# Kernel optimization log

Hardware: AMD Instinct MI355X
Metric: run time of the kernel (lower is better)

## Reference

```python
import jax, jax.numpy as jnp
import numpy as np

EPS = 1e-5
DIM, QK, PDIM, SR = 256, 64, 128, 2
B, H, W = 16, 64, 64
SCALE = QK ** (-0.5)


def _conv(x, w, stride, pad, groups=1):
    return jax.lax.conv_general_dilated(
        x, w, (stride, stride), [(pad, pad), (pad, pad)], feature_group_count=groups)


def _bn(x, g, b, m, v):
    # inference-mode BatchNorm2d with running stats
    s = (g / jnp.sqrt(v + EPS))[None, :, None, None]
    return (x - m[None, :, None, None]) * s + b[None, :, None, None]


def _gn1(x, g, b):
    # GroupNorm(1, C): normalize over (C,H,W) per sample
    mu = x.mean(axis=(1, 2, 3), keepdims=True)
    var = x.var(axis=(1, 2, 3), keepdims=True)
    xh = (x - mu) / jnp.sqrt(var + EPS)
    return xh * g[None, :, None, None] + b[None, :, None, None]


def setup_inputs() -> dict:
    key = jax.random.key(0)
    ks = jax.random.split(key, 6)
    inp = {
        'x': jax.random.normal(ks[0], (B, DIM, H, W), jnp.float32),
        'gn_g': jnp.ones((DIM,), jnp.float32),
        'gn_b': jnp.zeros((DIM,), jnp.float32),
        'w_in': jax.random.normal(ks[1], (2 * QK + DIM, DIM, 3, 3), jnp.float32) * 0.05,
        'bn_in_g': jnp.ones((2 * QK + DIM,), jnp.float32),
        'bn_in_b': jnp.zeros((2 * QK + DIM,), jnp.float32),
        'bn_in_m': jnp.zeros((2 * QK + DIM,), jnp.float32),
        'bn_in_v': jnp.ones((2 * QK + DIM,), jnp.float32),
        'w_k': jax.random.normal(ks[2], (QK, 1, SR, SR), jnp.float32) * 0.05,
        'bn_k_g': jnp.ones((QK,), jnp.float32),
        'bn_k_b': jnp.zeros((QK,), jnp.float32),
        'bn_k_m': jnp.zeros((QK,), jnp.float32),
        'bn_k_v': jnp.ones((QK,), jnp.float32),
        'w_v': jax.random.normal(ks[3], (PDIM, 1, SR, SR), jnp.float32) * 0.05,
        'bn_v_g': jnp.ones((PDIM,), jnp.float32),
        'bn_v_b': jnp.zeros((PDIM,), jnp.float32),
        'bn_v_m': jnp.zeros((PDIM,), jnp.float32),
        'bn_v_v': jnp.ones((PDIM,), jnp.float32),
        'w_out': jax.random.normal(ks[4], (DIM, DIM, 1, 1), jnp.float32) * 0.05,
        'bn_out_g': jnp.ones((DIM,), jnp.float32),
        'bn_out_b': jnp.zeros((DIM,), jnp.float32),
        'bn_out_m': jnp.zeros((DIM,), jnp.float32),
        'bn_out_v': jnp.ones((DIM,), jnp.float32),
    }
    return inp


def reference(x, gn_g, gn_b, w_in, bn_in_g, bn_in_b, bn_in_m, bn_in_v,
              w_k, bn_k_g, bn_k_b, bn_k_m, bn_k_v,
              w_v, bn_v_g, bn_v_b, bn_v_m, bn_v_v,
              w_out, bn_out_g, bn_out_b, bn_out_m, bn_out_v):
    x = _gn1(x, gn_g, gn_b)
    y = _bn(_conv(x, w_in, 1, 1), bn_in_g, bn_in_b, bn_in_m, bn_in_v)
    q = y[:, :QK]
    k = y[:, QK:2 * QK]
    v = y[:, 2 * QK:2 * QK + PDIM]
    u = y[:, 2 * QK + PDIM:]
    # depthwise sr-stride convs reduce k/v spatially
    k = _bn(_conv(k, w_k, SR, 0, groups=QK), bn_k_g, bn_k_b, bn_k_m, bn_k_v)
    v = _bn(_conv(v, w_v, SR, 0, groups=PDIM), bn_v_g, bn_v_b, bn_v_m, bn_v_v)
    b, _, h, w = u.shape
    qf = q.reshape(b, QK, -1)      # [B, QK, N]
    kf = k.reshape(b, QK, -1)      # [B, QK, M]
    vf = v.reshape(b, PDIM, -1)    # [B, PDIM, M]
    attn = jnp.einsum('bcn,bcm->bnm', qf, kf) * SCALE
    attn = jax.nn.softmax(attn, axis=-1)
    o = jnp.einsum('bcm,bnm->bcn', vf, attn).reshape(b, PDIM, h, w)
    cat = jnp.concatenate([o, u], axis=1)
    out = _bn(_conv(jax.nn.relu(cat), w_out, 1, 0), bn_out_g, bn_out_b, bn_out_m, bn_out_v)
    return out
```

## Files before the change

### kernel.cpp

```cpp
#include <hip/hip_runtime.h>
#include <stdint.h>

#define EPSV 1e-5f

typedef __attribute__((ext_vector_type(8))) short short8;
typedef __attribute__((ext_vector_type(4))) float f32x4;
typedef __bf16 bf16x8 __attribute__((ext_vector_type(8)));

__device__ __forceinline__ unsigned short f2bf(float f) {
  union { float f; unsigned int u; } v; v.f = f;
  unsigned int r = (v.u + 0x7FFFu + ((v.u >> 16) & 1u)) >> 16;
  return (unsigned short)r;
}
__device__ __forceinline__ float bf2f(unsigned short h) {
  union { unsigned int u; float f; } v; v.u = ((unsigned int)h) << 16;
  return v.f;
}

__device__ __forceinline__ f32x4 mfma16(bf16x8 a, bf16x8 b, f32x4 c) {
  return __builtin_amdgcn_mfma_f32_16x16x32_bf16(a, b, c, 0, 0, 0);
}

__device__ __forceinline__ unsigned cvt_pk_bf16(float lo, float hi) {
  unsigned r;
  asm("v_cvt_pk_bf16_f32 %0, %1, %2" : "=v"(r) : "v"(lo), "v"(hi));
  return r;
}

__device__ __forceinline__ bf16x8 dsread16(const unsigned short* p) {
  unsigned off = (unsigned)(uintptr_t)(const __attribute__((address_space(3))) unsigned short*)p;
  bf16x8 r;
  asm volatile("ds_read_b128 %0, %1" : "=v"(r) : "v"(off));
  return r;
}

#define GLOAD16(g, l)                                                          \
  __builtin_amdgcn_global_load_lds(                                            \
      (const __attribute__((address_space(1))) void*)(g),                      \
      (__attribute__((address_space(3))) void*)(l), 16, 0, 0)

__global__ __launch_bounds__(256) void k_gn_stats(const float* __restrict__ x,
                                                  float* __restrict__ stats) {
  int b = blockIdx.x >> 6, chunk = blockIdx.x & 63;
  const float4* xp = (const float4*)(x + ((size_t)b << 20) + (size_t)chunk * 16384);
  int t = threadIdx.x;
  float s = 0.f, q = 0.f;
#pragma unroll
  for (int i = 0; i < 16; ++i) {
    float4 v = xp[i * 256 + t];
    s += v.x + v.y + v.z + v.w;
    q += v.x * v.x + v.y * v.y + v.z * v.z + v.w * v.w;
  }
#pragma unroll
  for (int m = 1; m <= 32; m <<= 1) { s += __shfl_xor(s, m); q += __shfl_xor(q, m); }
  __shared__ float ls[8];
  int w = t >> 6, l = t & 63;
  if (l == 0) { ls[w * 2] = s; ls[w * 2 + 1] = q; }
  __syncthreads();
  if (t == 0) {
    float S = ls[0] + ls[2] + ls[4] + ls[6];
    float Q = ls[1] + ls[3] + ls[5] + ls[7];
    atomicAdd(&stats[b * 2], S);
    atomicAdd(&stats[b * 2 + 1], Q);
  }
}

__global__ __launch_bounds__(256) void k_gn_norm(const float* __restrict__ x,
                                                 const float* __restrict__ stats,
                                                 const float* __restrict__ g,
                                                 const float* __restrict__ bb,
                                                 unsigned short* __restrict__ xnp) {
  __shared__ float tile[64][65];
  int pt = blockIdx.x;
  int ct = blockIdx.y;
  int b = blockIdx.z;
  int t = threadIdx.x, tr = t >> 6, tc = t & 63;
  const float* xb = x + ((size_t)b << 20) + (size_t)(ct * 64) * 4096 + pt * 64;
#pragma unroll
  for (int i = 0; i < 16; ++i) {
    int r = i * 4 + tr;
    tile[r][tc] = xb[(size_t)r * 4096 + tc];
  }
  __syncthreads();
  float mu = stats[b * 2] * (1.f / 1048576.f);
  float var = stats[b * 2 + 1] * (1.f / 1048576.f) - mu * mu;
  float istd = rsqrtf(var + EPSV);
  float gg = g[ct * 64 + tc] * istd;
  float bv = bb[ct * 64 + tc];
  unsigned short* out = xnp + (((size_t)b * 66 + (pt + 1)) * 66 + 1) * 256 + ct * 64 + tc;
#pragma unroll
  for (int i = 0; i < 16; ++i) {
    int pcol = i * 4 + tr;
    float v = (tile[tc][pcol] - mu) * gg + bv;
    out[(size_t)pcol * 256] = f2bf(v);
  }
}

__global__ __launch_bounds__(256) void k_prep_wt(const float* __restrict__ w_in,
                                                 const float* __restrict__ bg,
                                                 const float* __restrict__ bv,
                                                 unsigned short* __restrict__ wt) {
  int idx = blockIdx.x * 256 + threadIdx.x;
  if (idx >= 9 * 384 * 256) return;
  int tap = idx / 98304;
  int rem = idx - tap * 98304;
  int co = rem >> 8, ci = rem & 255;
  float s = bg[co] * rsqrtf(bv[co] + EPSV);
  wt[idx] = f2bf(w_in[(size_t)(co * 256 + ci) * 9 + tap] * s);
}

__global__ __launch_bounds__(256) void k_prep_misc(
    const float* w_out, const float* og, const float* ob, const float* om, const float* ov,
    const float* big, const float* bib, const float* bim, const float* biv,
    const float* w_k, const float* kg, const float* kb, const float* km, const float* kvv,
    const float* w_v, const float* vg, const float* vb, const float* vm, const float* vvv,
    unsigned short* wo2, float* bias_in, float* bias_out,
    float* wkf, float* bias_k, float* wvf, float* bias_v) {
  int idx = blockIdx.x * 256 + threadIdx.x;
  if (idx < 65536) {
    int co = idx >> 8;
    float s = og[co] * rsqrtf(ov[co] + EPSV);
    wo2[idx] = f2bf(w_out[idx] * s);
    return;
  }
  idx -= 65536;
  if (idx < 384) {
    float s = big[idx] * rsqrtf(biv[idx] + EPSV);
    bias_in[idx] = bib[idx] - bim[idx] * s;
    return;
  }
  idx -= 384;
  if (idx < 256) {
    float s = og[idx] * rsqrtf(ov[idx] + EPSV);
    bias_out[idx] = ob[idx] - om[idx] * s;
    return;
  }
  idx -= 256;
  if (idx < 64) {
    float s = kg[idx] * rsqrtf(kvv[idx] + EPSV);
#pragma unroll
    for (int tp = 0; tp < 4; ++tp) wkf[idx * 4 + tp] = w_k[idx * 4 + tp] * s;
    bias_k[idx] = kb[idx] - km[idx] * s;
    return;
  }
  idx -= 64;
  if (idx < 128) {
    float s = vg[idx] * rsqrtf(vvv[idx] + EPSV);
#pragma unroll
    for (int tp = 0; tp < 4; ++tp) wvf[idx * 4 + tp] = w_v[idx * 4 + tp] * s;
    bias_v[idx] = vb[idx] - vm[idx] * s;
    return;
  }
}

__global__ __launch_bounds__(512, 2) void k_conv3(const unsigned short* __restrict__ xnp,
                                                  const unsigned short* __restrict__ wt,
                                                  const float* __restrict__ bias_in,
                                                  unsigned short* __restrict__ y) {
  __shared__ alignas(16) unsigned short As[2][256 * 64];
  __shared__ alignas(16) unsigned short Bs[2][192 * 64];
  int pt = blockIdx.x, cot = blockIdx.y, b = blockIdx.z;
  int p0 = pt * 256, co0 = cot * 192;
  int t = threadIdx.x, w = t >> 6, l = t & 63;
  int lg = l >> 4, lr = l & 15;
  int wrM = (w >> 2) * 128, wrN = (w & 3) * 48;

  int lchunk = (t & 7) ^ ((t >> 3) & 7);
  int abase[4];
#pragma unroll
  for (int i = 0; i < 4; ++i) {
    int row = (i * 512 + t) >> 3;
    int p = p0 + row;
    int yy = p >> 6, xx = p & 63;
    abase[i] = ((b * 66 + yy) * 66 + xx) * 256 + lchunk * 8;
  }
  int bbase[3];
#pragma unroll
  for (int i = 0; i < 3; ++i) {
    int row = (i * 512 + t) >> 3;
    bbase[i] = (co0 + row) * 256 + lchunk * 8;
  }

  f32x4 acc[8][3];
#pragma unroll
  for (int i = 0; i < 8; ++i)
#pragma unroll
    for (int j = 0; j < 3; ++j) acc[i][j] = f32x4{0.f, 0.f, 0.f, 0.f};

#define STAGE(step, buf)                                                       \
  do {                                                                         \
    int tap_ = (step) >> 2, kc_ = (step) & 3;                                  \
    int dy_ = (tap_ * 11) >> 5;                                                \
    int dx_ = tap_ - dy_ * 3;                                                  \
    int aoff_ = (dy_ * 66 + dx_) * 256 + kc_ * 64;                             \
    int boff_ = tap_ * 98304 + kc_ * 64;                                       \
    _Pragma("unroll")                                                          \
    for (int i_ = 0; i_ < 4; ++i_)                                             \
      GLOAD16(xnp + abase[i_] + aoff_, &As[buf][(i_ * 512 + w * 64) * 8]);     \
    _Pragma("unroll")                                                          \
    for (int i_ = 0; i_ < 3; ++i_)                                             \
      GLOAD16(wt + bbase[i_] + boff_, &Bs[buf][(i_ * 512 + w * 64) * 8]);      \
  } while (0)

  STAGE(0, 0);

  for (int step = 0; step < 36; ++step) {
    int cur = step & 1;
    asm volatile("" ::: "memory");
    if (step < 35) {
      STAGE(step + 1, cur ^ 1);
      asm volatile("s_waitcnt vmcnt(7)" ::: "memory");
    } else {
      asm volatile("s_waitcnt vmcnt(0)" ::: "memory");
    }
    __builtin_amdgcn_s_barrier();
    __builtin_amdgcn_sched_barrier(0);

    const unsigned short* Ac = As[cur];
    const unsigned short* Bc = Bs[cur];

    bf16x8 bfr[2][3];
#pragma unroll
    for (int k2 = 0; k2 < 2; ++k2)
#pragma unroll
      for (int nt = 0; nt < 3; ++nt) {
        int row = wrN + nt * 16 + lr;
        bfr[k2][nt] = dsread16(&Bc[row * 64 + (((k2 * 4 + lg) ^ (row & 7)) * 8)]);
      }
#pragma unroll
    for (int mh = 0; mh < 2; ++mh) {
      bf16x8 afr[4][2];
#pragma unroll
      for (int mt = 0; mt < 4; ++mt)
#pragma unroll
        for (int k2 = 0; k2 < 2; ++k2) {
          int row = wrM + mh * 64 + mt * 16 + lr;
          afr[mt][k2] = dsread16(&Ac[row * 64 + (((k2 * 4 + lg) ^ (row & 7)) * 8)]);
        }
      asm volatile("s_waitcnt lgkmcnt(0)" ::: "memory");
      __builtin_amdgcn_sched_barrier(0);
      __builtin_amdgcn_s_setprio(1);
#pragma unroll
      for (int mt = 0; mt < 4; ++mt)
#pragma unroll
        for (int nt = 0; nt < 3; ++nt) {
          acc[mh * 4 + mt][nt] = mfma16(afr[mt][0], bfr[0][nt], acc[mh * 4 + mt][nt]);
          acc[mh * 4 + mt][nt] = mfma16(afr[mt][1], bfr[1][nt], acc[mh * 4 + mt][nt]);
        }
      __builtin_amdgcn_s_setprio(0);
    }
    __builtin_amdgcn_sched_barrier(0);
    __builtin_amdgcn_s_barrier();
  }
#undef STAGE

  float bias[3];
#pragma unroll
  for (int nt = 0; nt < 3; ++nt) bias[nt] = bias_in[co0 + wrN + nt * 16 + lr];
#pragma unroll
  for (int m8 = 0; m8 < 8; ++m8) {
#pragma unroll
    for (int r = 0; r < 4; ++r) {
      int p = p0 + wrM + m8 * 16 + lg * 4 + r;
      size_t rowoff = ((size_t)(b * 4096 + p)) * 384;
#pragma unroll
      for (int nt = 0; nt < 3; ++nt) {
        int co = co0 + wrN + nt * 16 + lr;
        float v = acc[m8][nt][r] + bias[nt];
        if (co >= 256) v = fmaxf(v, 0.f);
        y[rowoff + co] = f2bf(v);
      }
    }
  }
}

__global__ __launch_bounds__(256) void k_kv(const unsigned short* __restrict__ y,
                                            const float* __restrict__ wkf, const float* __restrict__ bias_k,
                                            const float* __restrict__ wvf, const float* __restrict__ bias_v,
                                            unsigned short* __restrict__ kk, unsigned short* __restrict__ vv) {
  constexpr int LDW = 200;
  __shared__ unsigned short ty[128 * LDW];
  __shared__ unsigned short vt[128 * 33];
  int b = blockIdx.x >> 5, my = blockIdx.x & 31;
  int t = threadIdx.x;
  const unsigned short* ybase = y + ((size_t)(b * 4096 + my * 128)) * 384 + 64;
#pragma unroll
  for (int j = 0; j < 12; ++j) {
    int idx = j * 256 + t;
    int row = idx / 24, c8 = idx - row * 24;
    bf16x8 v = *(const bf16x8*)&ybase[(size_t)row * 384 + c8 * 8];
    *(bf16x8*)&ty[row * LDW + c8 * 8] = v;
  }
  __syncthreads();

  {
    int c = t & 63, wq = t >> 6;
    float wk0 = wkf[c * 4 + 0], wk1 = wkf[c * 4 + 1];
    float wk2 = wkf[c * 4 + 2], wk3 = wkf[c * 4 + 3];
    float bk = bias_k[c];
#pragma unroll
    for (int pass = 0; pass < 8; ++pass) {
      int mx = pass * 4 + wq;
      int r0 = 2 * mx, r1 = 2 * mx + 1;
      float a = bk;
      a += bf2f(ty[r0 * LDW + c]) * wk0;
      a += bf2f(ty[(r0 + 1) * LDW + c]) * wk1;
      a += bf2f(ty[(64 + r0) * LDW + c]) * wk2;
      a += bf2f(ty[(64 + r1) * LDW + c]) * wk3;
      kk[((size_t)(b * 1024 + my * 32 + mx)) * 64 + c] = f2bf(a);
    }
  }

  {
    int cv = t & 127, mxh = t >> 7;
    float wv0 = wvf[cv * 4 + 0], wv1 = wvf[cv * 4 + 1];
    float wv2 = wvf[cv * 4 + 2], wv3 = wvf[cv * 4 + 3];
    float bv = bias_v[cv];
    int col = 64 + cv;
#pragma unroll
    for (int pass = 0; pass < 16; ++pass) {
      int mx = pass * 2 + mxh;
      int r0 = 2 * mx, r1 = 2 * mx + 1;
      float a = bv;
      a += bf2f(ty[r0 * LDW + col]) * wv0;
      a += bf2f(ty[r1 * LDW + col]) * wv1;
      a += bf2f(ty[(64 + r0) * LDW + col]) * wv2;
      a += bf2f(ty[(64 + r1) * LDW + col]) * wv3;
      vt[cv * 33 + mx] = f2bf(a);
    }
  }
  __syncthreads();
  {
    int mx = t & 31, cvq = t >> 5;
#pragma unroll
    for (int i = 0; i < 16; ++i) {
      int cv = i * 8 + cvq;
      vv[((size_t)(b * 128 + cv)) * 1024 + my * 32 + mx] = vt[cv * 33 + mx];
    }
  }
}

__global__ __launch_bounds__(512, 4) void k_attn(unsigned short* __restrict__ y,
                                                 const unsigned short* __restrict__ kk,
                                                 const unsigned short* __restrict__ vvb) {
  __shared__ alignas(16) unsigned short Ks[2][4096];
  __shared__ alignas(16) unsigned short PT[8][64][16];
  int blk = blockIdx.x;
  int b = blk >> 5, ntile = blk & 31;
  int t = threadIdx.x, w = t >> 6, l = t & 63;
  int lg = l >> 4, lr = l & 15;
  int nq0 = ntile * 128 + w * 16;
  const float SC = 0.125f * 1.44269504f;

  union { short8 s; bf16x8 b; } uo;
#pragma unroll
  for (int i = 0; i < 8; ++i) uo.s[i] = (short)0x3F80;
  bf16x8 ones = uo.b;

  bf16x8 qf[2];
#pragma unroll
  for (int c = 0; c < 2; ++c)
    qf[c] = *(const bf16x8*)&y[((size_t)(b * 4096 + nq0 + lr)) * 384 + c * 32 + lg * 8];

  f32x4 oa[8];
#pragma unroll
  for (int tt = 0; tt < 8; ++tt) oa[tt] = f32x4{0.f, 0.f, 0.f, 0.f};
  float mi[4], li[4];
#pragma unroll
  for (int r = 0; r < 4; ++r) { mi[r] = -1e30f; li[r] = 0.f; }

  int srow = t >> 3;
  int skg = (t & 7) ^ (srow & 7);
  const unsigned short* ksrc = kk + ((size_t)(b * 1024 + srow)) * 64 + skg * 8;
  unsigned short* ldst0 = &Ks[0][w * 512];
  unsigned short* ldst1 = &Ks[1][w * 512];

  GLOAD16(ksrc, ldst0);
  __syncthreads();

  for (int it = 0; it < 16; ++it) {
    int cur = it & 1;
    const unsigned short* Kc = &Ks[cur][0];
    if (it < 15) GLOAD16(ksrc + (it + 1) * 4096, cur ? ldst0 : ldst1);

    f32x4 s[4];
#pragma unroll
    for (int mt = 0; mt < 4; ++mt) {
      int row = mt * 16 + lr;
      int sw = (lr & 7) << 3;
      bf16x8 kf0 = *(const bf16x8*)&Kc[row * 64 + ((lg * 8) ^ sw)];
      bf16x8 kf1 = *(const bf16x8*)&Kc[row * 64 + ((32 + lg * 8) ^ sw)];
      f32x4 z = f32x4{0.f, 0.f, 0.f, 0.f};
      z = mfma16(qf[0], kf0, z);
      z = mfma16(qf[1], kf1, z);
      s[mt] = z;
    }

    float rm[4];
#pragma unroll
    for (int r = 0; r < 4; ++r)
      rm[r] = fmaxf(fmaxf(s[0][r], s[1][r]), fmaxf(s[2][r], s[3][r]));
#pragma unroll
    for (int msk = 1; msk <= 8; msk <<= 1)
#pragma unroll
      for (int r = 0; r < 4; ++r) rm[r] = fmaxf(rm[r], __shfl_xor(rm[r], msk));
    bool grow = false;
#pragma unroll
    for (int r = 0; r < 4; ++r) grow |= (rm[r] * SC > mi[r]);
    if (__any(grow)) {
#pragma unroll
      for (int r = 0; r < 4; ++r) {
        float nm = fmaxf(mi[r], rm[r] * SC);
        float corr = exp2f(mi[r] - nm);
        mi[r] = nm;
        li[r] *= corr;
#pragma unroll
        for (int tt = 0; tt < 8; ++tt) oa[tt][r] *= corr;
      }
    }
#pragma unroll
    for (int mt = 0; mt < 4; ++mt)
#pragma unroll
      for (int r = 0; r < 4; ++r)
        s[mt][r] = exp2f(fmaf(s[mt][r], SC, -mi[r]));

#pragma unroll
    for (int mt = 0; mt < 4; ++mt) {
      unsigned p01 = cvt_pk_bf16(s[mt][0], s[mt][1]);
      unsigned p23 = cvt_pk_bf16(s[mt][2], s[mt][3]);
      unsigned long long pk = ((unsigned long long)p23 << 32) | p01;
      *(unsigned long long*)&PT[w][mt * 16 + lr][lg * 4] = pk;
    }
    asm volatile("s_waitcnt lgkmcnt(0)" ::: "memory");

    bf16x8 pf[2];
#pragma unroll
    for (int kc = 0; kc < 2; ++kc) {
      unsigned base = (unsigned)(uintptr_t)&PT[w][kc * 32 + lg * 8][lr];
      uint2 t0, t1;
      asm volatile("ds_read_b64_tr_b16 %0, %1" : "=v"(t0) : "v"(base));
      asm volatile("ds_read_b64_tr_b16 %0, %1 offset:128" : "=v"(t1) : "v"(base));
      union { unsigned u[4]; bf16x8 b; } cv;
      cv.u[0] = t0.x; cv.u[1] = t0.y; cv.u[2] = t1.x; cv.u[3] = t1.y;
      pf[kc] = cv.b;
    }
    asm volatile("s_waitcnt lgkmcnt(0)" ::: "memory");
    __builtin_amdgcn_sched_barrier(0);

    {
      f32x4 zz = f32x4{0.f, 0.f, 0.f, 0.f};
      zz = mfma16(pf[0], ones, zz);
      zz = mfma16(pf[1], ones, zz);
#pragma unroll
      for (int r = 0; r < 4; ++r) li[r] += zz[r];
    }

    size_t vbase = ((size_t)(b * 128)) * 1024 + it * 64 + lg * 8;
#pragma unroll
    for (int tt = 0; tt < 8; ++tt) {
      const unsigned short* vr = &vvb[vbase + (size_t)(tt * 16 + lr) * 1024];
      bf16x8 vf0 = *(const bf16x8*)&vr[0];
      bf16x8 vf1 = *(const bf16x8*)&vr[32];
      oa[tt] = mfma16(pf[0], vf0, oa[tt]);
      oa[tt] = mfma16(pf[1], vf1, oa[tt]);
    }
    __syncthreads();
  }

#pragma unroll
  for (int r = 0; r < 4; ++r) {
    float inv = 1.f / li[r];
    int p = nq0 + lg * 4 + r;
    size_t rowoff = ((size_t)(b * 4096 + p)) * 384 + 128;
#pragma unroll
    for (int tt = 0; tt < 8; ++tt) {
      float v = oa[tt][r] * inv;
      v = fmaxf(v, 0.f);
      y[rowoff + tt * 16 + lr] = f2bf(v);
    }
  }
}

__global__ __launch_bounds__(256) void k_conv1(const unsigned short* __restrict__ y,
                                               const unsigned short* __restrict__ wo2,
                                               const float* __restrict__ bias_out,
                                               float* __restrict__ out) {
  int ptile = blockIdx.x, cot = blockIdx.y, b = blockIdx.z;
  int p0 = ptile * 128, co0 = cot * 128;
  __shared__ alignas(16) unsigned short As[128 * 64];
  __shared__ alignas(16) unsigned short Bs[128 * 64];
  int t = threadIdx.x, w = t >> 6, l = t & 63;
  int rr = t >> 3, c8 = (t & 7) * 8;
  int lg = l >> 4, lr = l & 15;
  int baseA = (co0 + rr) * 256 + c8;
  size_t baseB = ((size_t)(b * 4096 + p0 + rr)) * 384 + 128 + c8;
  f32x4 acc[4][4];
#pragma unroll
  for (int i = 0; i < 4; ++i)
#pragma unroll
    for (int j = 0; j < 4; ++j) acc[i][j] = f32x4{0.f, 0.f, 0.f, 0.f};
  int wr = (w >> 1) * 64, wc = (w & 1) * 64;
#pragma unroll 1
  for (int kc = 0; kc < 4; ++kc) {
    int ci0 = kc * 64;
    __syncthreads();
#pragma unroll
    for (int i = 0; i < 4; ++i) {
      GLOAD16(wo2 + baseA + i * 8192 + ci0, &As[(i * 32 + w * 8) * 64]);
      GLOAD16(y + baseB + (size_t)i * 32 * 384 + ci0, &Bs[(i * 32 + w * 8) * 64]);
    }
    __syncthreads();
    bf16x8 af[4][2], bf[4][2];
#pragma unroll
    for (int mt = 0; mt < 4; ++mt)
#pragma unroll
      for (int k2 = 0; k2 < 2; ++k2) {
        af[mt][k2] = *(const bf16x8*)&As[(wr + mt * 16 + lr) * 64 + k2 * 32 + lg * 8];
        bf[mt][k2] = *(const bf16x8*)&Bs[(wc + mt * 16 + lr) * 64 + k2 * 32 + lg * 8];
      }
#pragma unroll
    for (int mt = 0; mt < 4; ++mt)
#pragma unroll
      for (int nt = 0; nt < 4; ++nt) {
        acc[mt][nt] = mfma16(af[mt][0], bf[nt][0], acc[mt][nt]);
        acc[mt][nt] = mfma16(af[mt][1], bf[nt][1], acc[mt][nt]);
      }
  }
#pragma unroll
  for (int mt = 0; mt < 4; ++mt)
#pragma unroll
    for (int r = 0; r < 4; ++r) {
      int co = co0 + wr + mt * 16 + lg * 4 + r;
      float bv = bias_out[co];
      size_t obase = ((size_t)(b * 256 + co)) << 12;
#pragma unroll
      for (int nt = 0; nt < 4; ++nt) {
        int p = p0 + wc + nt * 16 + lr;
        out[obase + p] = acc[mt][nt][r] + bv;
      }
    }
}

static constexpr size_t pad256(size_t x) { return (x + 255) & ~(size_t)255; }

extern "C" void kernel_launch(void* const* d_in, const int* in_sizes, int n_in,
                              void* d_out, int out_size, void* d_ws, size_t ws_size,
                              hipStream_t stream) {
  const float* x      = (const float*)d_in[0];
  const float* gn_g   = (const float*)d_in[1];
  const float* gn_b   = (const float*)d_in[2];
  const float* w_in   = (const float*)d_in[3];
  const float* bin_g  = (const float*)d_in[4];
  const float* bin_b  = (const float*)d_in[5];
  const float* bin_m  = (const float*)d_in[6];
  const float* bin_v  = (const float*)d_in[7];
  const float* w_k    = (const float*)d_in[8];
  const float* bk_g   = (const float*)d_in[9];
  const float* bk_b   = (const float*)d_in[10];
  const float* bk_m   = (const float*)d_in[11];
  const float* bk_v   = (const float*)d_in[12];
  const float* w_v    = (const float*)d_in[13];
  const float* bv_g   = (const float*)d_in[14];
  const float* bv_b   = (const float*)d_in[15];
  const float* bv_m   = (const float*)d_in[16];
  const float* bv_v   = (const float*)d_in[17];
  const float* w_out  = (const float*)d_in[18];
  const float* bo_g   = (const float*)d_in[19];
  const float* bo_b   = (const float*)d_in[20];
  const float* bo_m   = (const float*)d_in[21];
  const float* bo_v   = (const float*)d_in[22];
  float* out = (float*)d_out;

  char* ws = (char*)d_ws;
  size_t off = 0;
  float*          stats   = (float*)(ws + off);          off += pad256(128);
  unsigned short* wt      = (unsigned short*)(ws + off); off += pad256((size_t)9 * 384 * 256 * 2);
  float*          bias_in = (float*)(ws + off);          off += pad256(384 * 4);
  unsigned short* wo2     = (unsigned short*)(ws + off); off += pad256(256 * 256 * 2);
  float*          bias_out= (float*)(ws + off);          off += pad256(256 * 4);
  float*          wkf     = (float*)(ws + off);          off += pad256(64 * 4 * 4);
  float*          bias_k  = (float*)(ws + off);          off += pad256(64 * 4);
  float*          wvf     = (float*)(ws + off);          off += pad256(128 * 4 * 4);
  float*          bias_v  = (float*)(ws + off);          off += pad256(128 * 4);
  unsigned short* xnp     = (unsigned short*)(ws + off); off += pad256((size_t)16 * 66 * 66 * 256 * 2);
  unsigned short* y       = (unsigned short*)(ws + off); off += pad256((size_t)16 * 4096 * 384 * 2);
  unsigned short* kk      = (unsigned short*)(ws + off); off += pad256((size_t)16 * 1024 * 64 * 2);
  unsigned short* vv      = (unsigned short*)(ws + off); off += pad256((size_t)16 * 128 * 1024 * 2);
  (void)ws_size; (void)out_size; (void)n_in; (void)in_sizes;

  hipMemsetAsync(stats, 0, 256, stream);
  hipMemsetAsync(xnp, 0, (size_t)16 * 66 * 66 * 256 * 2, stream);

  k_gn_stats<<<1024, 256, 0, stream>>>(x, stats);
  k_prep_wt<<<3456, 256, 0, stream>>>(w_in, bin_g, bin_v, wt);
  k_prep_misc<<<260, 256, 0, stream>>>(w_out, bo_g, bo_b, bo_m, bo_v,
                                       bin_g, bin_b, bin_m, bin_v,
                                       w_k, bk_g, bk_b, bk_m, bk_v,
                                       w_v, bv_g, bv_b, bv_m, bv_v,
                                       wo2, bias_in, bias_out, wkf, bias_k, wvf, bias_v);
  k_gn_norm<<<dim3(64, 4, 16), 256, 0, stream>>>(x, stats, gn_g, gn_b, xnp);
  k_conv3<<<dim3(16, 2, 16), 512, 0, stream>>>(xnp, wt, bias_in, y);
  k_kv<<<512, 256, 0, stream>>>(y, wkf, bias_k, wvf, bias_v, kk, vv);
  k_attn<<<512, 512, 0, stream>>>(y, kk, vv);
  k_conv1<<<dim3(32, 2, 16), 256, 0, stream>>>(y, wo2, bias_out, out);
}
```

Measured before the change: 454.1 us.

## Shrink conv3 block tile to 128x192 with 4 waves and split-k LDS waits

The 3x3 conv implicit GEMM moves from 256-pixel tiles with 512 threads to 128-pixel tiles with 256 threads, doubling the grid to 1024 blocks. Each wave now computes a 64x96 sub-tile (4x6 MFMA tiles) instead of 128x48, and MFMAs on the first k-half start before the second half's LDS reads have landed. The aim is better CU fill, fewer LDS reads per MFMA, and overlap of LDS latency with compute. The cost is re-reading weight tiles across twice as many blocks and possible register pressure from 24 accumulators plus 20 fragments.

```diff
diff --git a/kernel.cpp b/kernel.cpp
--- a/kernel.cpp
+++ b/kernel.cpp
@@ -153,39 +153,39 @@
   }
 }
 
-__global__ __launch_bounds__(512, 2) void k_conv3(const unsigned short* __restrict__ xnp,
+__global__ __launch_bounds__(256, 2) void k_conv3(const unsigned short* __restrict__ xnp,
                                                   const unsigned short* __restrict__ wt,
                                                   const float* __restrict__ bias_in,
                                                   unsigned short* __restrict__ y) {
-  __shared__ alignas(16) unsigned short As[2][256 * 64];
+  __shared__ alignas(16) unsigned short As[2][128 * 64];
   __shared__ alignas(16) unsigned short Bs[2][192 * 64];
   int pt = blockIdx.x, cot = blockIdx.y, b = blockIdx.z;
-  int p0 = pt * 256, co0 = cot * 192;
+  int p0 = pt * 128, co0 = cot * 192;
   int t = threadIdx.x, w = t >> 6, l = t & 63;
   int lg = l >> 4, lr = l & 15;
-  int wrM = (w >> 2) * 128, wrN = (w & 3) * 48;
+  int wrM = (w >> 1) * 64, wrN = (w & 1) * 96;
 
   int lchunk = (t & 7) ^ ((t >> 3) & 7);
   int abase[4];
 #pragma unroll
   for (int i = 0; i < 4; ++i) {
-    int row = (i * 512 + t) >> 3;
+    int row = i * 32 + (t >> 3);
     int p = p0 + row;
     int yy = p >> 6, xx = p & 63;
     abase[i] = ((b * 66 + yy) * 66 + xx) * 256 + lchunk * 8;
   }
-  int bbase[3];
-#pragma unroll
-  for (int i = 0; i < 3; ++i) {
-    int row = (i * 512 + t) >> 3;
+  int bbase[6];
+#pragma unroll
+  for (int i = 0; i < 6; ++i) {
+    int row = i * 32 + (t >> 3);
     bbase[i] = (co0 + row) * 256 + lchunk * 8;
   }
 
-  f32x4 acc[8][3];
-#pragma unroll
-  for (int i = 0; i < 8; ++i)
-#pragma unroll
-    for (int j = 0; j < 3; ++j) acc[i][j] = f32x4{0.f, 0.f, 0.f, 0.f};
+  f32x4 acc[4][6];
+#pragma unroll
+  for (int i = 0; i < 4; ++i)
+#pragma unroll
+    for (int j = 0; j < 6; ++j) acc[i][j] = f32x4{0.f, 0.f, 0.f, 0.f};
 
 #define STAGE(step, buf)                                                       \
   do {                                                                         \
@@ -196,10 +196,10 @@
     int boff_ = tap_ * 98304 + kc_ * 64;                                       \
     _Pragma("unroll")                                                          \
     for (int i_ = 0; i_ < 4; ++i_)                                             \
-      GLOAD16(xnp + abase[i_] + aoff_, &As[buf][(i_ * 512 + w * 64) * 8]);     \
+      GLOAD16(xnp + abase[i_] + aoff_, &As[buf][(i_ * 256 + t) * 8]);          \
     _Pragma("unroll")                                                          \
-    for (int i_ = 0; i_ < 3; ++i_)                                             \
-      GLOAD16(wt + bbase[i_] + boff_, &Bs[buf][(i_ * 512 + w * 64) * 8]);      \
+    for (int i_ = 0; i_ < 6; ++i_)                                             \
+      GLOAD16(wt + bbase[i_] + boff_, &Bs[buf][(i_ * 256 + t) * 8]);           \
   } while (0)
 
   STAGE(0, 0);
@@ -209,7 +209,7 @@
     asm volatile("" ::: "memory");
     if (step < 35) {
       STAGE(step + 1, cur ^ 1);
-      asm volatile("s_waitcnt vmcnt(7)" ::: "memory");
+      asm volatile("s_waitcnt vmcnt(10)" ::: "memory");
     } else {
       asm volatile("s_waitcnt vmcnt(0)" ::: "memory");
     }
@@ -219,54 +219,56 @@
     const unsigned short* Ac = As[cur];
     const unsigned short* Bc = Bs[cur];
 
-    bf16x8 bfr[2][3];
-#pragma unroll
-    for (int k2 = 0; k2 < 2; ++k2)
-#pragma unroll
-      for (int nt = 0; nt < 3; ++nt) {
+    bf16x8 bfr[2][6], afr[2][4];
+#pragma unroll
+    for (int k2 = 0; k2 < 2; ++k2) {
+#pragma unroll
+      for (int nt = 0; nt < 6; ++nt) {
         int row = wrN + nt * 16 + lr;
         bfr[k2][nt] = dsread16(&Bc[row * 64 + (((k2 * 4 + lg) ^ (row & 7)) * 8)]);
       }
 #pragma unroll
-    for (int mh = 0; mh < 2; ++mh) {
-      bf16x8 afr[4][2];
-#pragma unroll
-      for (int mt = 0; mt < 4; ++mt)
-#pragma unroll
-        for (int k2 = 0; k2 < 2; ++k2) {
-          int row = wrM + mh * 64 + mt * 16 + lr;
-          afr[mt][k2] = dsread16(&Ac[row * 64 + (((k2 * 4 + lg) ^ (row & 7)) * 8)]);
-        }
-      asm volatile("s_waitcnt lgkmcnt(0)" ::: "memory");
-      __builtin_amdgcn_sched_barrier(0);
-      __builtin_amdgcn_s_setprio(1);
-#pragma unroll
-      for (int mt = 0; mt < 4; ++mt)
-#pragma unroll
-        for (int nt = 0; nt < 3; ++nt) {
-          acc[mh * 4 + mt][nt] = mfma16(afr[mt][0], bfr[0][nt], acc[mh * 4 + mt][nt]);
-          acc[mh * 4 + mt][nt] = mfma16(afr[mt][1], bfr[1][nt], acc[mh * 4 + mt][nt]);
-        }
-      __builtin_amdgcn_s_setprio(0);
-    }
+      for (int mt = 0; mt < 4; ++mt) {
+        int row = wrM + mt * 16 + lr;
+        afr[k2][mt] = dsread16(&Ac[row * 64 + (((k2 * 4 + lg) ^ (row & 7)) * 8)]);
+      }
+    }
+    asm volatile("s_waitcnt lgkmcnt(10)" ::: "memory");
+    __builtin_amdgcn_sched_barrier(0);
+    __builtin_amdgcn_s_setprio(1);
+#pragma unroll
+    for (int mt = 0; mt < 4; ++mt)
+#pragma unroll
+      for (int nt = 0; nt < 6; ++nt)
+        acc[mt][nt] = mfma16(afr[0][mt], bfr[0][nt], acc[mt][nt]);
+    __builtin_amdgcn_s_setprio(0);
+    asm volatile("s_waitcnt lgkmcnt(0)" ::: "memory");
+    __builtin_amdgcn_sched_barrier(0);
+    __builtin_amdgcn_s_setprio(1);
+#pragma unroll
+    for (int mt = 0; mt < 4; ++mt)
+#pragma unroll
+      for (int nt = 0; nt < 6; ++nt)
+        acc[mt][nt] = mfma16(afr[1][mt], bfr[1][nt], acc[mt][nt]);
+    __builtin_amdgcn_s_setprio(0);
     __builtin_amdgcn_sched_barrier(0);
     __builtin_amdgcn_s_barrier();
   }
 #undef STAGE
 
-  float bias[3];
-#pragma unroll
-  for (int nt = 0; nt < 3; ++nt) bias[nt] = bias_in[co0 + wrN + nt * 16 + lr];
-#pragma unroll
-  for (int m8 = 0; m8 < 8; ++m8) {
+  float bias[6];
+#pragma unroll
+  for (int nt = 0; nt < 6; ++nt) bias[nt] = bias_in[co0 + wrN + nt * 16 + lr];
+#pragma unroll
+  for (int mt = 0; mt < 4; ++mt) {
 #pragma unroll
     for (int r = 0; r < 4; ++r) {
-      int p = p0 + wrM + m8 * 16 + lg * 4 + r;
+      int p = p0 + wrM + mt * 16 + lg * 4 + r;
       size_t rowoff = ((size_t)(b * 4096 + p)) * 384;
 #pragma unroll
-      for (int nt = 0; nt < 3; ++nt) {
+      for (int nt = 0; nt < 6; ++nt) {
         int co = co0 + wrN + nt * 16 + lr;
-        float v = acc[m8][nt][r] + bias[nt];
+        float v = acc[mt][nt][r] + bias[nt];
         if (co >= 256) v = fmaxf(v, 0.f);
         y[rowoff + co] = f2bf(v);
       }
@@ -599,7 +601,7 @@
                                        w_v, bv_g, bv_b, bv_m, bv_v,
                                        wo2, bias_in, bias_out, wkf, bias_k, wvf, bias_v);
   k_gn_norm<<<dim3(64, 4, 16), 256, 0, stream>>>(x, stats, gn_g, gn_b, xnp);
-  k_conv3<<<dim3(16, 2, 16), 512, 0, stream>>>(xnp, wt, bias_in, y);
+  k_conv3<<<dim3(32, 2, 16), 256, 0, stream>>>(xnp, wt, bias_in, y);
   k_kv<<<512, 256, 0, stream>>>(y, wkf, bias_k, wvf, bias_v, kk, vv);
   k_attn<<<512, 512, 0, stream>>>(y, kk, vv);
   k_conv1<<<dim3(32, 2, 16), 256, 0, stream>>>(y, wo2, bias_out, out);
```

After: 438.4 us. 1.04x faster.
